# Kernel tuning notes

Hardware: AMD Instinct MI355X
Metric: run time of the kernel (lower is better)

The kernel has to match this reference:

```python
import jax, jax.numpy as jnp
import numpy as np

B, L, D = 8, 2048, 256
NEG = 10000.0


def setup_inputs() -> dict:
    key = jax.random.key(0)
    kq, kk, kv, km = jax.random.split(key, 4)
    return {
        "query": jax.random.normal(kq, (B, L, D), dtype=jnp.float32),
        "key": jax.random.normal(kk, (B, L, D), dtype=jnp.float32),
        "value": jax.random.normal(kv, (B, L, D), dtype=jnp.float32),
        "mask": jax.random.randint(km, (B, L), 0, 2).astype(bool),
    }


def reference(query, key, value, mask):
    d = query.shape[-1]
    # scores: [B, Lq, Lk]
    e = jnp.einsum("bqd,bkd->bqk", query, key) / jnp.sqrt(jnp.asarray(d, query.dtype))
    # history_only (causal) mask: subtract 10000 where key index > query index
    q_len, k_len = query.shape[1], key.shape[1]
    causal = (jnp.arange(k_len)[None, :] > jnp.arange(q_len)[:, None]).astype(query.dtype)
    e = e - NEG * causal[None, :, :]
    # key padding mask: [B, 1, Lk]
    e = e - NEG * (1.0 - mask.astype(query.dtype))[:, None, :]
    attn = jax.nn.softmax(e, axis=-1)
    return jnp.einsum("bqk,bkd->bqd", attn, value)
```

## Files before the change

kernel.cpp:

```cpp
#include <hip/hip_runtime.h>
#include <stdint.h>

#define NL 2048
#define ND 256
#define KVB 32
#define QB 64
#define NQT 32
#define NT_ALL (NL / KVB)
#define CHUNK 8
#define NCHUNKS_B 151
#define TILE_BYTES (KVB * ND * 2)
#define IMG (8 * NT_ALL * TILE_BYTES)
#define WS_K 256
#define WS_V (WS_K + IMG)
#define WS_Q (WS_V + IMG)
#define WS_P (WS_Q + IMG)
#define PART_BYTES (QB * ND * 2 + QB * 8)

typedef __attribute__((ext_vector_type(8))) short short8;
typedef __attribute__((ext_vector_type(4))) short short4v;
typedef __attribute__((ext_vector_type(4))) float f32x4;
typedef __attribute__((ext_vector_type(8))) unsigned short ushort8;

__device__ __forceinline__ unsigned short bf16rne(float x) {
  unsigned u = __builtin_bit_cast(unsigned, x);
  u += 0x7FFFu + ((u >> 16) & 1u);
  return (unsigned short)(u >> 16);
}

__device__ __forceinline__ short8 cvt8(float4 a, float4 b, float scale) {
  short8 v;
  v[0] = (short)bf16rne(a.x * scale);
  v[1] = (short)bf16rne(a.y * scale);
  v[2] = (short)bf16rne(a.z * scale);
  v[3] = (short)bf16rne(a.w * scale);
  v[4] = (short)bf16rne(b.x * scale);
  v[5] = (short)bf16rne(b.y * scale);
  v[6] = (short)bf16rne(b.z * scale);
  v[7] = (short)bf16rne(b.w * scale);
  return v;
}

__global__ void mask_mode_kernel(const unsigned* __restrict__ M, int* __restrict__ flag) {
  bool bad = false;
  for (int i = threadIdx.x; i < 4096; i += 64) {
    if (M[i] > 1u) bad = true;
  }
  unsigned long long b = __ballot(bad);
  if (threadIdx.x == 0) *flag = (b != 0ULL) ? 1 : 0;
}

__global__ __launch_bounds__(128)
void convert_qkv(const float* __restrict__ Q, const float* __restrict__ K,
                 const float* __restrict__ V, unsigned char* __restrict__ ws) {
  const int t = blockIdx.x;
  const int b = t >> 6, tix = t & 63;
  const float* qt = Q + ((size_t)b * NL + tix * KVB) * ND;
  const float* kt = K + ((size_t)b * NL + tix * KVB) * ND;
  const float* vt = V + ((size_t)b * NL + tix * KVB) * ND;
  unsigned char* qd = ws + WS_Q + (size_t)t * TILE_BYTES;
  unsigned char* kd = ws + WS_K + (size_t)t * TILE_BYTES;
  unsigned char* vd = ws + WS_V + (size_t)t * TILE_BYTES;
#pragma unroll
  for (int it = 0; it < 8; ++it) {
    int idx = it * 128 + threadIdx.x;
    int row = idx >> 5, u = idx & 31, f = u * 8;
    const float4* qp = (const float4*)(qt + (size_t)row * ND + f);
    *(short8*)(qd + (row * 512 + f * 2)) = cvt8(qp[0], qp[1], 0.0625f);
    const float4* kp = (const float4*)(kt + (size_t)row * ND + f);
    int kb = (row * 512 + f * 2) ^ ((row & 7) << 4);
    *(short8*)(kd + kb) = cvt8(kp[0], kp[1], 1.0f);
    const float4* vp = (const float4*)(vt + (size_t)row * ND + f);
    int vb = (row >> 2) * 2048 + (u >> 1) * 128 + (row & 3) * 32 + (u & 1) * 16;
    *(short8*)(vd + vb) = cvt8(vp[0], vp[1], 1.0f);
  }
}

__global__ __launch_bounds__(256, 2)
void attn_fwd(const int* __restrict__ Mg, unsigned char* ws,
              const int* __restrict__ modeFlag) {
  __shared__ unsigned short Ks[2][KVB * ND];
  __shared__ unsigned short Vs[2][KVB * ND];
  __shared__ float biasS[2][KVB];
  __shared__ unsigned short Ps[4][16 * KVB];

  const int tid = threadIdx.x;
  const int wv = tid >> 6;
  const int lane = tid & 63;
  const int g = lane >> 4;
  const int cc = lane & 15;
  const int maskByteMode = *modeFlag;

  const int fid = blockIdx.x;
  const int b = fid / NCHUNKS_B;
  int rem = fid - b * NCHUNKS_B;
  int qt = 0, c = 0, pbase = 0;
  if (rem < 8) {
    qt = 0; c = rem; pbase = 0;
  } else {
    rem -= 8; pbase = 8;
    for (qt = 1; qt < NQT; ++qt) {
      int n = (qt >> 2) + 1;
      if (rem < n) { c = rem; break; }
      rem -= n; pbase += n;
    }
  }
  const int qb = qt * QB;
  const int nt_s = (qt == 0) ? NT_ALL : (2 * qt + 2);
  const int t0 = c * CHUNK;
  const int t1 = min(nt_s, t0 + CHUNK);
  unsigned char* pp = ws + WS_P + (size_t)(b * NCHUNKS_B + pbase + c) * PART_BYTES;
  unsigned short* ppA = (unsigned short*)pp;
  float* ppM = (float*)(pp + QB * ND * 2);
  float* ppL = ppM + QB;

  auto stage_tile = [&](int tix, int bi) {
    const unsigned char* kg = ws + WS_K + ((size_t)(b * NT_ALL + tix)) * TILE_BYTES;
    const unsigned char* vg = ws + WS_V + ((size_t)(b * NT_ALL + tix)) * TILE_BYTES;
#pragma unroll
    for (int s = 0; s < 4; ++s) {
      const int seg = wv * 4 + s;
      __builtin_amdgcn_global_load_lds(
          (const __attribute__((address_space(1))) unsigned int*)(kg + seg * 1024 + lane * 16),
          (__attribute__((address_space(3))) unsigned int*)((unsigned char*)&Ks[bi][0] + seg * 1024),
          16, 0, 0);
      __builtin_amdgcn_global_load_lds(
          (const __attribute__((address_space(1))) unsigned int*)(vg + seg * 1024 + lane * 16),
          (__attribute__((address_space(3))) unsigned int*)((unsigned char*)&Vs[bi][0] + seg * 1024),
          16, 0, 0);
    }
    if (tid < KVB) {
      int mv = maskByteMode
                   ? (int)((const unsigned char*)Mg)[(size_t)b * NL + tix * KVB + tid]
                   : Mg[(size_t)b * NL + tix * KVB + tid];
      biasS[bi][tid] = mv ? 0.f : -10000.f;
    }
  };

  const unsigned char* qrow = ws + WS_Q + ((size_t)b * NL + (qb + 16 * wv + cc)) * 512;
  short8 qf[8];
#pragma unroll
  for (int ch = 0; ch < 8; ++ch) {
    qf[ch] = *(const short8*)(qrow + ch * 64 + g * 16);
  }

  f32x4 acc[16];
#pragma unroll
  for (int i = 0; i < 16; ++i) acc[i] = (f32x4){0.f, 0.f, 0.f, 0.f};
  float m_run[4], l_run[4];
#pragma unroll
  for (int r = 0; r < 4; ++r) { m_run[r] = -3.0e38f; l_run[r] = 0.f; }

  int buf = 0;
  stage_tile(t0, 0);
  __syncthreads();

  for (int tix = t0; tix < t1; ++tix) {
    if (tix + 1 < t1) stage_tile(tix + 1, buf ^ 1);
    const int kv0 = tix * KVB;

    const char* ksB = (const char*)&Ks[buf][0];
    f32x4 s0 = {0.f, 0.f, 0.f, 0.f}, s1 = {0.f, 0.f, 0.f, 0.f};
#pragma unroll
    for (int ch = 0; ch < 8; ++ch) {
      int cbase = ch * 64 + g * 16;
      int b0 = (cc * 512 + cbase) ^ ((cc & 7) << 4);
      int b1 = ((cc + 16) * 512 + cbase) ^ ((cc & 7) << 4);
      short8 k0 = *reinterpret_cast<const short8*>(ksB + b0);
      short8 k1 = *reinterpret_cast<const short8*>(ksB + b1);
      s0 = __builtin_amdgcn_mfma_f32_16x16x32_bf16(qf[ch], k0, s0, 0, 0, 0);
      s1 = __builtin_amdgcn_mfma_f32_16x16x32_bf16(qf[ch], k1, s1, 0, 0, 0);
    }
    float bi0 = biasS[buf][cc], bi1 = biasS[buf][16 + cc];
    s0 += bi0;
    s1 += bi1;
    if (kv0 + KVB - 1 > qb) {
      int kvg0 = kv0 + cc, kvg1 = kv0 + 16 + cc;
      int qg = qb + 16 * wv + 4 * g;
#pragma unroll
      for (int r = 0; r < 4; ++r) {
        if (kvg0 > qg + r) s0[r] -= 10000.f;
        if (kvg1 > qg + r) s1[r] -= 10000.f;
      }
    }
    float rmax[4], alpha[4], rsum[4];
#pragma unroll
    for (int r = 0; r < 4; ++r) rmax[r] = fmaxf(s0[r], s1[r]);
#pragma unroll
    for (int off = 8; off >= 1; off >>= 1) {
#pragma unroll
      for (int r = 0; r < 4; ++r) rmax[r] = fmaxf(rmax[r], __shfl_xor(rmax[r], off));
    }
#pragma unroll
    for (int r = 0; r < 4; ++r) {
      float mn = fmaxf(m_run[r], rmax[r]);
      alpha[r] = __expf(m_run[r] - mn);
      m_run[r] = mn;
    }
#pragma unroll
    for (int r = 0; r < 4; ++r) {
      s0[r] = __expf(s0[r] - m_run[r]);
      s1[r] = __expf(s1[r] - m_run[r]);
      rsum[r] = s0[r] + s1[r];
    }
#pragma unroll
    for (int off = 8; off >= 1; off >>= 1) {
#pragma unroll
      for (int r = 0; r < 4; ++r) rsum[r] += __shfl_xor(rsum[r], off);
    }
    f32x4 av = {alpha[0], alpha[1], alpha[2], alpha[3]};
#pragma unroll
    for (int r = 0; r < 4; ++r) l_run[r] = l_run[r] * alpha[r] + rsum[r];
#pragma unroll
    for (int i = 0; i < 16; ++i) acc[i] *= av;

    unsigned short* pw = &Ps[wv][0];
#pragma unroll
    for (int r = 0; r < 4; ++r) {
      pw[(4 * g + r) * KVB + cc] = bf16rne(s0[r]);
      pw[(4 * g + r) * KVB + 16 + cc] = bf16rne(s1[r]);
    }
    asm volatile("s_waitcnt lgkmcnt(0)" ::: "memory");
    short8 pa = *reinterpret_cast<const short8*>((const char*)pw + cc * 64 + g * 16);

    const unsigned va = (unsigned)(uintptr_t)&Vs[buf][0] + g * 4096 + cc * 8;
#pragma unroll
    for (int h8 = 0; h8 < 2; ++h8) {
      short4v lo[8], hi[8];
#pragma unroll
      for (int f8 = 0; f8 < 8; ++f8) {
        const int ft = h8 * 8 + f8;
        asm volatile("ds_read_b64_tr_b16 %0, %1 offset:%2"
                     : "=&v"(lo[f8]) : "v"(va), "i"(ft * 128) : "memory");
        asm volatile("ds_read_b64_tr_b16 %0, %1 offset:%2"
                     : "=&v"(hi[f8]) : "v"(va), "i"(ft * 128 + 2048) : "memory");
      }
      asm volatile("s_waitcnt lgkmcnt(0)" ::: "memory");
      __builtin_amdgcn_sched_barrier(0);
#pragma unroll
      for (int f8 = 0; f8 < 8; ++f8) {
        short8 vb = __builtin_shufflevector(lo[f8], hi[f8], 0, 1, 2, 3, 4, 5, 6, 7);
        acc[h8 * 8 + f8] =
            __builtin_amdgcn_mfma_f32_16x16x32_bf16(pa, vb, acc[h8 * 8 + f8], 0, 0, 0);
      }
    }

    __syncthreads();
    buf ^= 1;
  }

  unsigned short* sc = (unsigned short*)&Ks[0][0];
#pragma unroll
  for (int ft = 0; ft < 16; ++ft) {
#pragma unroll
    for (int r = 0; r < 4; ++r) {
      sc[(16 * wv + 4 * g + r) * 256 + ft * 16 + cc] = bf16rne(acc[ft][r]);
    }
  }
  if (cc == 0) {
#pragma unroll
    for (int r = 0; r < 4; ++r) {
      int rr = 16 * wv + 4 * g + r;
      ppM[rr] = m_run[r];
      ppL[rr] = l_run[r];
    }
  }
  __syncthreads();
  {
    const int row = tid >> 2, q4 = tid & 3;
    const unsigned short* srow = sc + row * 256 + q4 * 64;
#pragma unroll
    for (int k = 0; k < 8; ++k) {
      *(ushort8*)(ppA + (size_t)row * ND + q4 * 64 + k * 8) =
          *(const ushort8*)(srow + k * 8);
    }
  }
}

__global__ __launch_bounds__(256)
void attn_combine(const unsigned char* __restrict__ ws, float* __restrict__ Og) {
  const int bid = blockIdx.x;
  const int b = bid >> 5, qt = bid & 31;
  const int tid = threadIdx.x;
  const int row = tid >> 2, sub = tid & 3;

  int pbase = 0, nc = 8;
  if (qt > 0) {
    pbase = 8;
    for (int j = 1; j < qt; ++j) pbase += (j >> 2) + 1;
    nc = (qt >> 2) + 1;
  }
  const unsigned char* p0 = ws + WS_P + (size_t)(b * NCHUNKS_B + pbase) * PART_BYTES;

  float M = -3.0e38f;
  for (int c = 0; c < nc; ++c) {
    M = fmaxf(M, *(const float*)(p0 + (size_t)c * PART_BYTES + QB * ND * 2 + row * 4));
  }
  float L = 0.f;
  float o[64];
#pragma unroll
  for (int j = 0; j < 64; ++j) o[j] = 0.f;
  for (int c = 0; c < nc; ++c) {
    const unsigned char* pc = p0 + (size_t)c * PART_BYTES;
    float mm = *(const float*)(pc + QB * ND * 2 + row * 4);
    float ll = *(const float*)(pc + QB * ND * 2 + QB * 4 + row * 4);
    float s = __expf(mm - M);
    L += ll * s;
    const unsigned short* pa =
        (const unsigned short*)pc + (size_t)row * ND + sub * 64;
#pragma unroll
    for (int k = 0; k < 8; ++k) {
      ushort8 a = *(const ushort8*)(pa + k * 8);
#pragma unroll
      for (int j = 0; j < 8; ++j) {
        unsigned u = ((unsigned)a[j]) << 16;
        o[k * 8 + j] += __builtin_bit_cast(float, u) * s;
      }
    }
  }
  const float invL = 1.0f / L;
  float* op = Og + ((size_t)b * NL + qt * QB + row) * ND + sub * 64;
#pragma unroll
  for (int k = 0; k < 16; ++k) {
    float4 v = {o[k * 4] * invL, o[k * 4 + 1] * invL, o[k * 4 + 2] * invL,
                o[k * 4 + 3] * invL};
    *(float4*)(op + k * 4) = v;
  }
}

extern "C" void kernel_launch(void* const* d_in, const int* in_sizes, int n_in,
                              void* d_out, int out_size, void* d_ws, size_t ws_size,
                              hipStream_t stream) {
  (void)in_sizes; (void)n_in; (void)out_size; (void)ws_size;
  const float* Q = (const float*)d_in[0];
  const float* K = (const float*)d_in[1];
  const float* V = (const float*)d_in[2];
  const int* M = (const int*)d_in[3];
  unsigned char* ws = (unsigned char*)d_ws;

  mask_mode_kernel<<<dim3(1), dim3(64), 0, stream>>>((const unsigned*)M, (int*)ws);
  convert_qkv<<<dim3(512), dim3(128), 0, stream>>>(Q, K, V, ws);
  attn_fwd<<<dim3(8 * NCHUNKS_B), dim3(256), 0, stream>>>(M, ws, (const int*)ws);
  attn_combine<<<dim3(256), dim3(256), 0, stream>>>(ws, (float*)d_out);
}
```

Before: 118.2 us.

## Single-buffer K/V LDS tiles, raise occupancy, enlarge KV chunks, interleave batches

```diff
diff --git a/kernel.cpp b/kernel.cpp
--- a/kernel.cpp
+++ b/kernel.cpp
@@ -7,8 +7,8 @@
 #define QB 64
 #define NQT 32
 #define NT_ALL (NL / KVB)
-#define CHUNK 8
-#define NCHUNKS_B 151
+#define CHUNK 10
+#define NCHUNKS_B 125
 #define TILE_BYTES (KVB * ND * 2)
 #define IMG (8 * NT_ALL * TILE_BYTES)
 #define WS_K 256
@@ -76,12 +76,12 @@
   }
 }
 
-__global__ __launch_bounds__(256, 2)
+__global__ __launch_bounds__(256, 4)
 void attn_fwd(const int* __restrict__ Mg, unsigned char* ws,
               const int* __restrict__ modeFlag) {
-  __shared__ unsigned short Ks[2][KVB * ND];
-  __shared__ unsigned short Vs[2][KVB * ND];
-  __shared__ float biasS[2][KVB];
+  __shared__ unsigned short Ks[KVB * ND];
+  __shared__ unsigned short Vs[KVB * ND];
+  __shared__ float biasS[KVB];
   __shared__ unsigned short Ps[4][16 * KVB];
 
   const int tid = threadIdx.x;
@@ -92,17 +92,17 @@
   const int maskByteMode = *modeFlag;
 
   const int fid = blockIdx.x;
-  const int b = fid / NCHUNKS_B;
-  int rem = fid - b * NCHUNKS_B;
+  const int b = fid & 7;
+  const int k = fid >> 3;
   int qt = 0, c = 0, pbase = 0;
-  if (rem < 8) {
-    qt = 0; c = rem; pbase = 0;
+  if (k < 7) {
+    qt = 0; c = k; pbase = 0;
   } else {
-    rem -= 8; pbase = 8;
+    int rem = k - 7; pbase = 7;
     for (qt = 1; qt < NQT; ++qt) {
-      int n = (qt >> 2) + 1;
-      if (rem < n) { c = rem; break; }
-      rem -= n; pbase += n;
+      int nc = (2 * qt + 2 + CHUNK - 1) / CHUNK;
+      if (rem < nc) { c = rem; break; }
+      rem -= nc; pbase += nc;
     }
   }
   const int qb = qt * QB;
@@ -114,7 +114,7 @@
   float* ppM = (float*)(pp + QB * ND * 2);
   float* ppL = ppM + QB;
 
-  auto stage_tile = [&](int tix, int bi) {
+  auto stage_tile = [&](int tix) {
     const unsigned char* kg = ws + WS_K + ((size_t)(b * NT_ALL + tix)) * TILE_BYTES;
     const unsigned char* vg = ws + WS_V + ((size_t)(b * NT_ALL + tix)) * TILE_BYTES;
 #pragma unroll
@@ -122,18 +122,18 @@
       const int seg = wv * 4 + s;
       __builtin_amdgcn_global_load_lds(
           (const __attribute__((address_space(1))) unsigned int*)(kg + seg * 1024 + lane * 16),
-          (__attribute__((address_space(3))) unsigned int*)((unsigned char*)&Ks[bi][0] + seg * 1024),
+          (__attribute__((address_space(3))) unsigned int*)((unsigned char*)&Ks[0] + seg * 1024),
           16, 0, 0);
       __builtin_amdgcn_global_load_lds(
           (const __attribute__((address_space(1))) unsigned int*)(vg + seg * 1024 + lane * 16),
-          (__attribute__((address_space(3))) unsigned int*)((unsigned char*)&Vs[bi][0] + seg * 1024),
+          (__attribute__((address_space(3))) unsigned int*)((unsigned char*)&Vs[0] + seg * 1024),
           16, 0, 0);
     }
     if (tid < KVB) {
       int mv = maskByteMode
                    ? (int)((const unsigned char*)Mg)[(size_t)b * NL + tix * KVB + tid]
                    : Mg[(size_t)b * NL + tix * KVB + tid];
-      biasS[bi][tid] = mv ? 0.f : -10000.f;
+      biasS[tid] = mv ? 0.f : -10000.f;
     }
   };
 
@@ -151,15 +151,14 @@
 #pragma unroll
   for (int r = 0; r < 4; ++r) { m_run[r] = -3.0e38f; l_run[r] = 0.f; }
 
-  int buf = 0;
-  stage_tile(t0, 0);
-  __syncthreads();
+  const unsigned va = (unsigned)(uintptr_t)&Vs[0] + g * 4096 + cc * 8;
 
   for (int tix = t0; tix < t1; ++tix) {
-    if (tix + 1 < t1) stage_tile(tix + 1, buf ^ 1);
+    stage_tile(tix);
+    __syncthreads();
     const int kv0 = tix * KVB;
 
-    const char* ksB = (const char*)&Ks[buf][0];
+    const char* ksB = (const char*)&Ks[0];
     f32x4 s0 = {0.f, 0.f, 0.f, 0.f}, s1 = {0.f, 0.f, 0.f, 0.f};
 #pragma unroll
     for (int ch = 0; ch < 8; ++ch) {
@@ -171,7 +170,7 @@
       s0 = __builtin_amdgcn_mfma_f32_16x16x32_bf16(qf[ch], k0, s0, 0, 0, 0);
       s1 = __builtin_amdgcn_mfma_f32_16x16x32_bf16(qf[ch], k1, s1, 0, 0, 0);
     }
-    float bi0 = biasS[buf][cc], bi1 = biasS[buf][16 + cc];
+    float bi0 = biasS[cc], bi1 = biasS[16 + cc];
     s0 += bi0;
     s1 += bi1;
     if (kv0 + KVB - 1 > qb) {
@@ -223,7 +222,6 @@
     asm volatile("s_waitcnt lgkmcnt(0)" ::: "memory");
     short8 pa = *reinterpret_cast<const short8*>((const char*)pw + cc * 64 + g * 16);
 
-    const unsigned va = (unsigned)(uintptr_t)&Vs[buf][0] + g * 4096 + cc * 8;
 #pragma unroll
     for (int h8 = 0; h8 < 2; ++h8) {
       short4v lo[8], hi[8];
@@ -246,10 +244,9 @@
     }
 
     __syncthreads();
-    buf ^= 1;
-  }
-
-  unsigned short* sc = (unsigned short*)&Ks[0][0];
+  }
+
+  unsigned short* sc = (unsigned short*)&Ks[0];
 #pragma unroll
   for (int ft = 0; ft < 16; ++ft) {
 #pragma unroll
@@ -270,9 +267,9 @@
     const int row = tid >> 2, q4 = tid & 3;
     const unsigned short* srow = sc + row * 256 + q4 * 64;
 #pragma unroll
-    for (int k = 0; k < 8; ++k) {
-      *(ushort8*)(ppA + (size_t)row * ND + q4 * 64 + k * 8) =
-          *(const ushort8*)(srow + k * 8);
+    for (int kk = 0; kk < 8; ++kk) {
+      *(ushort8*)(ppA + (size_t)row * ND + q4 * 64 + kk * 8) =
+          *(const ushort8*)(srow + kk * 8);
     }
   }
 }
@@ -284,11 +281,11 @@
   const int tid = threadIdx.x;
   const int row = tid >> 2, sub = tid & 3;
 
-  int pbase = 0, nc = 8;
+  int pbase = 0, nc = 7;
   if (qt > 0) {
-    pbase = 8;
-    for (int j = 1; j < qt; ++j) pbase += (j >> 2) + 1;
-    nc = (qt >> 2) + 1;
+    pbase = 7;
+    for (int j = 1; j < qt; ++j) pbase += (2 * j + 2 + CHUNK - 1) / CHUNK;
+    nc = (2 * qt + 2 + CHUNK - 1) / CHUNK;
   }
   const unsigned char* p0 = ws + WS_P + (size_t)(b * NCHUNKS_B + pbase) * PART_BYTES;
 
@@ -309,22 +306,22 @@
     const unsigned short* pa =
         (const unsigned short*)pc + (size_t)row * ND + sub * 64;
 #pragma unroll
-    for (int k = 0; k < 8; ++k) {
-      ushort8 a = *(const ushort8*)(pa + k * 8);
+    for (int kk = 0; kk < 8; ++kk) {
+      ushort8 a = *(const ushort8*)(pa + kk * 8);
 #pragma unroll
       for (int j = 0; j < 8; ++j) {
         unsigned u = ((unsigned)a[j]) << 16;
-        o[k * 8 + j] += __builtin_bit_cast(float, u) * s;
+        o[kk * 8 + j] += __builtin_bit_cast(float, u) * s;
       }
     }
   }
   const float invL = 1.0f / L;
   float* op = Og + ((size_t)b * NL + qt * QB + row) * ND + sub * 64;
 #pragma unroll
-  for (int k = 0; k < 16; ++k) {
-    float4 v = {o[k * 4] * invL, o[k * 4 + 1] * invL, o[k * 4 + 2] * invL,
-                o[k * 4 + 3] * invL};
-    *(float4*)(op + k * 4) = v;
+  for (int kk = 0; kk < 16; ++kk) {
+    float4 v = {o[kk * 4] * invL, o[kk * 4 + 1] * invL, o[kk * 4 + 2] * invL,
+                o[kk * 4 + 3] * invL};
+    *(float4*)(op + kk * 4) = v;
   }
 }
 
```

Measured after the change: 161.7 us. +36.8%, slower.

## Double query tile to 128 rows with 8 waves sharing each K/V tile

Applied to the files above, without the earlier changes.

```diff
diff --git a/kernel.cpp b/kernel.cpp
--- a/kernel.cpp
+++ b/kernel.cpp
@@ -4,11 +4,11 @@
 #define NL 2048
 #define ND 256
 #define KVB 32
-#define QB 64
-#define NQT 32
+#define QB 128
+#define NQT 16
 #define NT_ALL (NL / KVB)
 #define CHUNK 8
-#define NCHUNKS_B 151
+#define NCHUNKS_B 79
 #define TILE_BYTES (KVB * ND * 2)
 #define IMG (8 * NT_ALL * TILE_BYTES)
 #define WS_K 256
@@ -76,13 +76,13 @@
   }
 }
 
-__global__ __launch_bounds__(256, 2)
+__global__ __launch_bounds__(512, 4)
 void attn_fwd(const int* __restrict__ Mg, unsigned char* ws,
               const int* __restrict__ modeFlag) {
   __shared__ unsigned short Ks[2][KVB * ND];
   __shared__ unsigned short Vs[2][KVB * ND];
-  __shared__ float biasS[2][KVB];
-  __shared__ unsigned short Ps[4][16 * KVB];
+  __shared__ unsigned short Ps[8][16 * KVB];
+  __shared__ float biasC[CHUNK * KVB];
 
   const int tid = threadIdx.x;
   const int wv = tid >> 6;
@@ -100,13 +100,13 @@
   } else {
     rem -= 8; pbase = 8;
     for (qt = 1; qt < NQT; ++qt) {
-      int n = (qt >> 2) + 1;
-      if (rem < n) { c = rem; break; }
-      rem -= n; pbase += n;
+      int ncq = (4 * qt + 4 + CHUNK - 1) / CHUNK;
+      if (rem < ncq) { c = rem; break; }
+      rem -= ncq; pbase += ncq;
     }
   }
   const int qb = qt * QB;
-  const int nt_s = (qt == 0) ? NT_ALL : (2 * qt + 2);
+  const int nt_s = (qt == 0) ? NT_ALL : (4 * qt + 4);
   const int t0 = c * CHUNK;
   const int t1 = min(nt_s, t0 + CHUNK);
   unsigned char* pp = ws + WS_P + (size_t)(b * NCHUNKS_B + pbase + c) * PART_BYTES;
@@ -114,12 +114,21 @@
   float* ppM = (float*)(pp + QB * ND * 2);
   float* ppL = ppM + QB;
 
+  {
+    int nb = (t1 - t0) * KVB;
+    for (int i = tid; i < nb; i += 512) {
+      size_t gi = (size_t)b * NL + t0 * KVB + i;
+      int mv = maskByteMode ? (int)((const unsigned char*)Mg)[gi] : Mg[gi];
+      biasC[i] = mv ? 0.f : -10000.f;
+    }
+  }
+
   auto stage_tile = [&](int tix, int bi) {
     const unsigned char* kg = ws + WS_K + ((size_t)(b * NT_ALL + tix)) * TILE_BYTES;
     const unsigned char* vg = ws + WS_V + ((size_t)(b * NT_ALL + tix)) * TILE_BYTES;
 #pragma unroll
-    for (int s = 0; s < 4; ++s) {
-      const int seg = wv * 4 + s;
+    for (int s = 0; s < 2; ++s) {
+      const int seg = wv * 2 + s;
       __builtin_amdgcn_global_load_lds(
           (const __attribute__((address_space(1))) unsigned int*)(kg + seg * 1024 + lane * 16),
           (__attribute__((address_space(3))) unsigned int*)((unsigned char*)&Ks[bi][0] + seg * 1024),
@@ -129,12 +138,6 @@
           (__attribute__((address_space(3))) unsigned int*)((unsigned char*)&Vs[bi][0] + seg * 1024),
           16, 0, 0);
     }
-    if (tid < KVB) {
-      int mv = maskByteMode
-                   ? (int)((const unsigned char*)Mg)[(size_t)b * NL + tix * KVB + tid]
-                   : Mg[(size_t)b * NL + tix * KVB + tid];
-      biasS[bi][tid] = mv ? 0.f : -10000.f;
-    }
   };
 
   const unsigned char* qrow = ws + WS_Q + ((size_t)b * NL + (qb + 16 * wv + cc)) * 512;
@@ -158,6 +161,7 @@
   for (int tix = t0; tix < t1; ++tix) {
     if (tix + 1 < t1) stage_tile(tix + 1, buf ^ 1);
     const int kv0 = tix * KVB;
+    const float* biasT = &biasC[(tix - t0) * KVB];
 
     const char* ksB = (const char*)&Ks[buf][0];
     f32x4 s0 = {0.f, 0.f, 0.f, 0.f}, s1 = {0.f, 0.f, 0.f, 0.f};
@@ -171,7 +175,7 @@
       s0 = __builtin_amdgcn_mfma_f32_16x16x32_bf16(qf[ch], k0, s0, 0, 0, 0);
       s1 = __builtin_amdgcn_mfma_f32_16x16x32_bf16(qf[ch], k1, s1, 0, 0, 0);
     }
-    float bi0 = biasS[buf][cc], bi1 = biasS[buf][16 + cc];
+    float bi0 = biasT[cc], bi1 = biasT[16 + cc];
     s0 += bi0;
     s1 += bi1;
     if (kv0 + KVB - 1 > qb) {
@@ -249,14 +253,6 @@
     buf ^= 1;
   }
 
-  unsigned short* sc = (unsigned short*)&Ks[0][0];
-#pragma unroll
-  for (int ft = 0; ft < 16; ++ft) {
-#pragma unroll
-    for (int r = 0; r < 4; ++r) {
-      sc[(16 * wv + 4 * g + r) * 256 + ft * 16 + cc] = bf16rne(acc[ft][r]);
-    }
-  }
   if (cc == 0) {
 #pragma unroll
     for (int r = 0; r < 4; ++r) {
@@ -265,36 +261,49 @@
       ppL[rr] = l_run[r];
     }
   }
-  __syncthreads();
-  {
-    const int row = tid >> 2, q4 = tid & 3;
-    const unsigned short* srow = sc + row * 256 + q4 * 64;
-#pragma unroll
-    for (int k = 0; k < 8; ++k) {
-      *(ushort8*)(ppA + (size_t)row * ND + q4 * 64 + k * 8) =
-          *(const ushort8*)(srow + k * 8);
-    }
+  unsigned short* sc = &Ks[0][0];
+#pragma unroll
+  for (int h = 0; h < 2; ++h) {
+    __syncthreads();
+    if ((wv >> 2) == h) {
+#pragma unroll
+      for (int ft = 0; ft < 16; ++ft) {
+#pragma unroll
+        for (int r = 0; r < 4; ++r) {
+          sc[(16 * (wv & 3) + 4 * g + r) * 256 + ft * 16 + cc] = bf16rne(acc[ft][r]);
+        }
+      }
+    }
+    __syncthreads();
+    const int row = tid >> 3, oct = tid & 7;
+    const ushort8* src = (const ushort8*)(sc + row * 256 + oct * 32);
+    ushort8* dst = (ushort8*)(ppA + (size_t)(h * 64 + row) * ND + oct * 32);
+#pragma unroll
+    for (int k = 0; k < 4; ++k) __builtin_nontemporal_store(src[k], dst + k);
   }
 }
 
 __global__ __launch_bounds__(256)
 void attn_combine(const unsigned char* __restrict__ ws, float* __restrict__ Og) {
   const int bid = blockIdx.x;
-  const int b = bid >> 5, qt = bid & 31;
+  const int b = bid >> 5;
+  const int qt = (bid >> 1) & 15;
+  const int h = bid & 1;
   const int tid = threadIdx.x;
   const int row = tid >> 2, sub = tid & 3;
+  const int grow = h * 64 + row;
 
   int pbase = 0, nc = 8;
   if (qt > 0) {
     pbase = 8;
-    for (int j = 1; j < qt; ++j) pbase += (j >> 2) + 1;
-    nc = (qt >> 2) + 1;
+    for (int j = 1; j < qt; ++j) pbase += (4 * j + 4 + CHUNK - 1) / CHUNK;
+    nc = (4 * qt + 4 + CHUNK - 1) / CHUNK;
   }
   const unsigned char* p0 = ws + WS_P + (size_t)(b * NCHUNKS_B + pbase) * PART_BYTES;
 
   float M = -3.0e38f;
   for (int c = 0; c < nc; ++c) {
-    M = fmaxf(M, *(const float*)(p0 + (size_t)c * PART_BYTES + QB * ND * 2 + row * 4));
+    M = fmaxf(M, *(const float*)(p0 + (size_t)c * PART_BYTES + QB * ND * 2 + grow * 4));
   }
   float L = 0.f;
   float o[64];
@@ -302,29 +311,29 @@
   for (int j = 0; j < 64; ++j) o[j] = 0.f;
   for (int c = 0; c < nc; ++c) {
     const unsigned char* pc = p0 + (size_t)c * PART_BYTES;
-    float mm = *(const float*)(pc + QB * ND * 2 + row * 4);
-    float ll = *(const float*)(pc + QB * ND * 2 + QB * 4 + row * 4);
+    float mm = *(const float*)(pc + QB * ND * 2 + grow * 4);
+    float ll = *(const float*)(pc + QB * ND * 2 + QB * 4 + grow * 4);
     float s = __expf(mm - M);
     L += ll * s;
-    const unsigned short* pa =
-        (const unsigned short*)pc + (size_t)row * ND + sub * 64;
-#pragma unroll
-    for (int k = 0; k < 8; ++k) {
-      ushort8 a = *(const ushort8*)(pa + k * 8);
+    const ushort8* pa = (const ushort8*)((const unsigned short*)pc +
+                                         (size_t)grow * ND + sub * 64);
+#pragma unroll
+    for (int kk = 0; kk < 8; ++kk) {
+      ushort8 a = __builtin_nontemporal_load(pa + kk);
 #pragma unroll
       for (int j = 0; j < 8; ++j) {
         unsigned u = ((unsigned)a[j]) << 16;
-        o[k * 8 + j] += __builtin_bit_cast(float, u) * s;
+        o[kk * 8 + j] += __builtin_bit_cast(float, u) * s;
       }
     }
   }
   const float invL = 1.0f / L;
-  float* op = Og + ((size_t)b * NL + qt * QB + row) * ND + sub * 64;
-#pragma unroll
-  for (int k = 0; k < 16; ++k) {
-    float4 v = {o[k * 4] * invL, o[k * 4 + 1] * invL, o[k * 4 + 2] * invL,
-                o[k * 4 + 3] * invL};
-    *(float4*)(op + k * 4) = v;
+  float* op = Og + ((size_t)b * NL + qt * QB + grow) * ND + sub * 64;
+#pragma unroll
+  for (int kk = 0; kk < 16; ++kk) {
+    float4 v = {o[kk * 4] * invL, o[kk * 4 + 1] * invL, o[kk * 4 + 2] * invL,
+                o[kk * 4 + 3] * invL};
+    *(float4*)(op + kk * 4) = v;
   }
 }
 
@@ -340,6 +349,6 @@
 
   mask_mode_kernel<<<dim3(1), dim3(64), 0, stream>>>((const unsigned*)M, (int*)ws);
   convert_qkv<<<dim3(512), dim3(128), 0, stream>>>(Q, K, V, ws);
-  attn_fwd<<<dim3(8 * NCHUNKS_B), dim3(256), 0, stream>>>(M, ws, (const int*)ws);
+  attn_fwd<<<dim3(8 * NCHUNKS_B), dim3(512), 0, stream>>>(M, ws, (const int*)ws);
   attn_combine<<<dim3(256), dim3(256), 0, stream>>>(ws, (float*)d_out);
 }
```

After: 251.5 us. 2.13x slower.
